# Performance work log

Measured on AMD Instinct MI355X. Metric: run time of the kernel, lower is better.

## Reference

```python
import jax, jax.numpy as jnp
import numpy as np

D_MODEL = 1024
N_HEADS = 16
D_HEAD = 64

def setup_inputs() -> dict:
    key = jax.random.key(0)
    k_x, k_q, k_k, k_v, k_o = jax.random.split(key, 5)
    B, T = 2, 2048
    scale = 1.0 / np.sqrt(D_MODEL)
    x = jax.random.normal(k_x, (B, T, D_MODEL), dtype=jnp.float32)
    W_q = jax.random.normal(k_q, (D_MODEL, N_HEADS * D_HEAD), dtype=jnp.float32) * scale
    W_k = jax.random.normal(k_k, (D_MODEL, N_HEADS * D_HEAD), dtype=jnp.float32) * scale
    W_v = jax.random.normal(k_v, (D_MODEL, N_HEADS * D_HEAD), dtype=jnp.float32) * scale
    W_out = jax.random.normal(k_o, (N_HEADS * D_HEAD, D_MODEL), dtype=jnp.float32) * scale
    return {"x": x, "W_q": W_q, "W_k": W_k, "W_v": W_v, "W_out": W_out}

def reference(x, W_q, W_k, W_v, W_out):
    B, T, _ = x.shape
    # project and split heads: [B, T, H, D] -> [B, H, T, D]
    def heads(W):
        return (x @ W).reshape(B, T, N_HEADS, D_HEAD).transpose(0, 2, 1, 3)
    Q, K, V = heads(W_q), heads(W_k), heads(W_v)
    scores = jnp.einsum('bhqd,bhkd->bhqk', Q, K) / jnp.sqrt(jnp.float32(D_HEAD))
    causal = jnp.tril(jnp.ones((T, T), dtype=bool))  # True = keep
    scores = jnp.where(causal, scores, jnp.float32(-jnp.inf))
    attn = jax.nn.softmax(scores, axis=-1)
    z = jnp.einsum('bhqk,bhkd->bhqd', attn, V)
    z = z.transpose(0, 2, 1, 3).reshape(B, T, N_HEADS * D_HEAD)
    return z @ W_out
```

## Files before the change

kernel.cpp:

```cpp
#include <hip/hip_runtime.h>
#include <cstdint>
#include <cstddef>

typedef __bf16 bf16_t;
typedef __bf16 bf16x8 __attribute__((ext_vector_type(8)));
typedef __bf16 bf16x4 __attribute__((ext_vector_type(4)));
typedef float floatx4 __attribute__((ext_vector_type(4)));

#define MFMA_BF16_16x16x32(a, b, c) \
  __builtin_amdgcn_mfma_f32_16x16x32_bf16((a), (b), (c), 0, 0, 0)

static constexpr int kT = 2048;
static constexpr int kDM = 1024;
static constexpr int kNH = 16;
static constexpr int kDH = 64;
static constexpr float kLog2e = 1.4426950408889634f;
static constexpr int kPS = 140;

__device__ __forceinline__ void gl_lds16(const bf16_t* g, bf16_t* l) {
  __builtin_amdgcn_global_load_lds(
      (const __attribute__((address_space(1))) void*)g,
      (__attribute__((address_space(3))) void*)l, 16, 0, 0);
}

__global__ __launch_bounds__(256) void detect_dtype(
    const unsigned short* __restrict__ xv, int* __restrict__ flagp) {
  __shared__ int bad_s[256];
  int bad = 0;
  for (int i = threadIdx.x; i < 8192; i += 256) {
    const unsigned e = (xv[i] >> 7) & 0xFF;
    if (e == 0xFF || (e != 0 && (e < 107 || e > 147))) bad++;
  }
  bad_s[threadIdx.x] = bad;
  __syncthreads();
  for (int s = 128; s > 0; s >>= 1) {
    if (threadIdx.x < s) bad_s[threadIdx.x] += bad_s[threadIdx.x + s];
    __syncthreads();
  }
  if (threadIdx.x == 0) *flagp = (bad_s[0] * 10 < 8192) ? 1 : 0;
}

__global__ __launch_bounds__(256) void convert_x(
    const void* __restrict__ src, bf16_t* __restrict__ dst,
    const int* __restrict__ flagp, int n) {
  const int f = *flagp;
  const int i = (blockIdx.x * 256 + threadIdx.x) * 8;
  if (i >= n) return;
  if (f) {
    *(bf16x8*)(dst + i) = *(const bf16x8*)((const bf16_t*)src + i);
  } else {
    const float* s = (const float*)src + i;
    bf16x8 v;
#pragma unroll
    for (int j = 0; j < 8; j++) v[j] = (bf16_t)s[j];
    *(bf16x8*)(dst + i) = v;
  }
}

__global__ __launch_bounds__(256) void convert_transpose_w(
    const void* __restrict__ w0, const void* __restrict__ w1,
    const void* __restrict__ w2, const void* __restrict__ w3,
    bf16_t* __restrict__ out_base, const int* __restrict__ flagp) {
  const int f = *flagp;
  const void* src = (blockIdx.z == 0) ? w0
                  : (blockIdx.z == 1) ? w1
                  : (blockIdx.z == 2) ? w2 : w3;
  bf16_t* dst = out_base + (size_t)blockIdx.z * (kDM * kDM);
  __shared__ bf16_t tile[64][65];
  const int tx = threadIdx.x & 63;
  const int ty = threadIdx.x >> 6;
  const int x0 = blockIdx.x * 64;
  const int y0 = blockIdx.y * 64;
#pragma unroll
  for (int r = 0; r < 64; r += 4) {
    const size_t idx = (size_t)(y0 + ty + r) * kDM + x0 + tx;
    tile[ty + r][tx] =
        f ? ((const bf16_t*)src)[idx] : (bf16_t)((const float*)src)[idx];
  }
  __syncthreads();
#pragma unroll
  for (int r = 0; r < 64; r += 4)
    dst[(size_t)(x0 + ty + r) * kDM + y0 + tx] = tile[tx][ty + r];
}

__device__ __forceinline__ void gemm_core_128x128(
    const bf16_t* __restrict__ A, const bf16_t* __restrict__ Bt, int K,
    bf16_t* __restrict__ sA, bf16_t* __restrict__ sB, floatx4 acc[4][4]) {
  const int tid = threadIdx.x;
  const int lane = tid & 63;
  const int w = tid >> 6;
  const int quad = lane >> 4;
  const int l16 = lane & 15;
  const int wm = w >> 1;
  const int wn = w & 1;
  const int sr = tid >> 2;
  const int sc = (tid & 3) * 8;
  const int wbase = w * 512;

  const bf16_t* pa0 = A + (size_t)sr * K + sc;
  const bf16_t* pa1 = A + (size_t)(sr + 64) * K + sc;
  const bf16_t* pb0 = Bt + (size_t)sr * K + sc;
  const bf16_t* pb1 = Bt + (size_t)(sr + 64) * K + sc;

  for (int kk = 0; kk < K; kk += 32) {
    __syncthreads();
    gl_lds16(pa0 + kk, sA + wbase);
    gl_lds16(pa1 + kk, sA + 2048 + wbase);
    gl_lds16(pb0 + kk, sB + wbase);
    gl_lds16(pb1 + kk, sB + 2048 + wbase);
    __syncthreads();
    bf16x8 af[4], bf[4];
#pragma unroll
    for (int mi = 0; mi < 4; mi++)
      af[mi] = *(const bf16x8*)(sA + (wm * 64 + mi * 16 + l16) * 32 + quad * 8);
#pragma unroll
    for (int ni = 0; ni < 4; ni++)
      bf[ni] = *(const bf16x8*)(sB + (wn * 64 + ni * 16 + l16) * 32 + quad * 8);
#pragma unroll
    for (int mi = 0; mi < 4; mi++)
#pragma unroll
      for (int ni = 0; ni < 4; ni++)
        acc[mi][ni] = MFMA_BF16_16x16x32(af[mi], bf[ni], acc[mi][ni]);
  }
}

__device__ __forceinline__ void gemm_core_64x128(
    const bf16_t* __restrict__ A, const bf16_t* __restrict__ Bt, int K,
    bf16_t* __restrict__ sA, bf16_t* __restrict__ sB, floatx4 acc[2][4]) {
  const int tid = threadIdx.x;
  const int lane = tid & 63;
  const int w = tid >> 6;
  const int quad = lane >> 4;
  const int l16 = lane & 15;
  const int wm = w >> 1;
  const int wn = w & 1;
  const int sr = tid >> 2;
  const int sc = (tid & 3) * 8;
  const int wbase = w * 512;

  const bf16_t* pa = A + (size_t)sr * K + sc;
  const bf16_t* pb0 = Bt + (size_t)sr * K + sc;
  const bf16_t* pb1 = Bt + (size_t)(sr + 64) * K + sc;

  for (int kk = 0; kk < K; kk += 32) {
    __syncthreads();
    gl_lds16(pa + kk, sA + wbase);
    gl_lds16(pb0 + kk, sB + wbase);
    gl_lds16(pb1 + kk, sB + 2048 + wbase);
    __syncthreads();
    bf16x8 af[2], bf[4];
#pragma unroll
    for (int mi = 0; mi < 2; mi++)
      af[mi] = *(const bf16x8*)(sA + (wm * 32 + mi * 16 + l16) * 32 + quad * 8);
#pragma unroll
    for (int ni = 0; ni < 4; ni++)
      bf[ni] = *(const bf16x8*)(sB + (wn * 64 + ni * 16 + l16) * 32 + quad * 8);
#pragma unroll
    for (int mi = 0; mi < 2; mi++)
#pragma unroll
      for (int ni = 0; ni < 4; ni++)
        acc[mi][ni] = MFMA_BF16_16x16x32(af[mi], bf[ni], acc[mi][ni]);
  }
}

__global__ __launch_bounds__(256) void qkv_proj(
    const bf16_t* __restrict__ x, const bf16_t* __restrict__ wt_base,
    bf16_t* __restrict__ Qf, bf16_t* __restrict__ Kf, bf16_t* __restrict__ Vf) {
  __shared__ bf16_t smem[8704];
  const int n0 = blockIdx.x * 128;
  const int m0 = blockIdx.y * 128;
  const int which = blockIdx.z;
  const bf16_t* Bt = wt_base + (size_t)which * (kDM * kDM);

  floatx4 acc[4][4];
  const floatx4 zero4 = {0.f, 0.f, 0.f, 0.f};
#pragma unroll
  for (int mi = 0; mi < 4; mi++)
#pragma unroll
    for (int ni = 0; ni < 4; ni++) acc[mi][ni] = zero4;

  gemm_core_128x128(x + (size_t)m0 * kDM, Bt + (size_t)n0 * kDM, kDM,
                    smem, smem + 4096, acc);

  const int tid = threadIdx.x;
  const int lane = tid & 63, w = tid >> 6;
  const int quad = lane >> 4, l16 = lane & 15;
  const int wm = w >> 1, wn = w & 1;
  const int h = (n0 + wn * 64) >> 6;

  if (which == 2) {
#pragma unroll
    for (int mi = 0; mi < 4; mi++) {
#pragma unroll
      for (int ni = 0; ni < 4; ni++) {
        const int n = n0 + wn * 64 + ni * 16 + l16;
        const int d = n & 63;
        const int ndv = d >> 4, l16v = d & 15;
        const int m = m0 + wm * 64 + mi * 16 + quad * 4;
        const int b = m >> 11, t0 = m & (kT - 1);
        const int kt = t0 >> 7, ks = (t0 >> 5) & 3, quadv = (t0 >> 3) & 3;
        const int eb = t0 & 4;
        bf16x4 v;
        v[0] = (bf16_t)acc[mi][ni][0];
        v[1] = (bf16_t)acc[mi][ni][1];
        v[2] = (bf16_t)acc[mi][ni][2];
        v[3] = (bf16_t)acc[mi][ni][3];
        *(bf16x4*)(Vf + (((((size_t)(b * kNH + h) * 16 + kt) * 4 + ks) * 4 +
                          ndv) * 64 + quadv * 16 + l16v) * 8 + eb) = v;
      }
    }
  } else {
    __syncthreads();
    bf16_t* Out = (which == 0) ? Qf : Kf;
    bf16_t* Lw = smem + w * 2176;
#pragma unroll
    for (int pass = 0; pass < 2; pass++) {
#pragma unroll
      for (int mi2 = 0; mi2 < 2; mi2++) {
        const int mi = pass * 2 + mi2;
#pragma unroll
        for (int ni = 0; ni < 4; ni++)
#pragma unroll
          for (int reg = 0; reg < 4; reg++)
            Lw[(mi2 * 16 + quad * 4 + reg) * 68 + ni * 16 + l16] =
                (bf16_t)acc[mi][ni][reg];
      }
      __asm volatile("s_waitcnt lgkmcnt(0)" ::: "memory");
      const int tb = m0 + wm * 64 + pass * 32;
#pragma unroll
      for (int i = 0; i < 4; i++) {
        const int khf = i >> 1, nifr = i & 1;
        const bf16x8 v = *(const bf16x8*)(Lw + (nifr * 16 + l16) * 68 +
                                          khf * 32 + quad * 8);
        const int t0 = tb + nifr * 16;
        const int b = t0 >> 11, tt = t0 & (kT - 1);
        size_t base;
        if (which == 0) {
          base = (((size_t)(b * kNH + h) * 128 + (tt >> 4)) * 2 + khf) * 512;
        } else {
          const int kt = tt >> 7, nif = (tt & 127) >> 4;
          base = ((((size_t)(b * kNH + h) * 16 + kt) * 2 + khf) * 8 + nif) * 512;
        }
        *(bf16x8*)(Out + base + lane * 8) = v;
      }
    }
  }
}

__device__ __forceinline__ void attn_task(
    int task, int lane, int l16, int quad, const bf16_t* __restrict__ Qb,
    const bf16_t* __restrict__ Kbf, const bf16_t* __restrict__ Vbf,
    bf16_t* __restrict__ Pw, bf16_t* __restrict__ Z, int b, int h) {
  const int q0 = task * 16;
  const int nkt = (task >> 3) + 1;
  const float C1 = 0.125f * kLog2e;

  bf16x8 qf[2];
#pragma unroll
  for (int kh = 0; kh < 2; kh++)
    qf[kh] = *(const bf16x8*)(Qb + ((size_t)task * 2 + kh) * 512 + lane * 8);

  const floatx4 zero4 = {0.f, 0.f, 0.f, 0.f};
  floatx4 of[4];
  float lrow[4];
#pragma unroll
  for (int nd = 0; nd < 4; nd++) of[nd] = zero4;
#pragma unroll
  for (int r = 0; r < 4; r++) lrow[r] = 0.f;

  bf16x8 kf[16];
#pragma unroll
  for (int fi = 0; fi < 16; fi++)
    kf[fi] = *(const bf16x8*)(Kbf + (size_t)fi * 512 + lane * 8);

  for (int kt = 0; kt < nkt; kt++) {
    const int kbase = kt * 128;
    floatx4 sf[8];
#pragma unroll
    for (int ni = 0; ni < 8; ni++) sf[ni] = zero4;
#pragma unroll
    for (int kh = 0; kh < 2; kh++)
#pragma unroll
      for (int ni = 0; ni < 8; ni++)
        sf[ni] = MFMA_BF16_16x16x32(qf[kh], kf[kh * 8 + ni], sf[ni]);
    const int ktp = (kt + 1 < nkt) ? kt + 1 : kt;
    const bf16_t* kp = Kbf + (size_t)ktp * 16 * 512 + lane * 8;
#pragma unroll
    for (int fi = 0; fi < 16; fi++)
      kf[fi] = *(const bf16x8*)(kp + (size_t)fi * 512);
    const bf16_t* vp = Vbf + (size_t)kt * 16 * 512 + lane * 8;
    bf16x8 vf[16];
#pragma unroll
    for (int fi = 0; fi < 16; fi++)
      vf[fi] = *(const bf16x8*)(vp + (size_t)fi * 512);
    const bool diag = (kt == nkt - 1);
#pragma unroll
    for (int reg = 0; reg < 4; reg++) {
      const int row_l = quad * 4 + reg;
      const int row_g = q0 + row_l;
      float rsum = 0.f;
#pragma unroll
      for (int ni = 0; ni < 8; ni++) {
        float s = sf[ni][reg] * C1 - 16.f;
        if (diag && (kbase + ni * 16 + l16 > row_g)) s = -3.0e38f;
        const float p = exp2f(s);
        rsum += p;
        Pw[row_l * kPS + ni * 16 + l16] = (bf16_t)p;
      }
      lrow[reg] += rsum;
    }
    __asm volatile("s_waitcnt lgkmcnt(0)" ::: "memory");
#pragma unroll
    for (int ks = 0; ks < 4; ks++) {
      const bf16x8 af = *(const bf16x8*)(Pw + l16 * kPS + ks * 32 + quad * 8);
#pragma unroll
      for (int nd = 0; nd < 4; nd++)
        of[nd] = MFMA_BF16_16x16x32(af, vf[ks * 4 + nd], of[nd]);
    }
  }

#pragma unroll
  for (int reg = 0; reg < 4; reg++) {
#pragma unroll
    for (int off = 1; off < 16; off <<= 1)
      lrow[reg] += __shfl_xor(lrow[reg], off, 64);
  }
#pragma unroll
  for (int reg = 0; reg < 4; reg++) {
    const int t = q0 + quad * 4 + reg;
    const float inv = 1.f / lrow[reg];
#pragma unroll
    for (int nd = 0; nd < 4; nd++) {
      const int col = h * 64 + nd * 16 + l16;
      Z[(size_t)(b * kT + t) * kDM + col] = (bf16_t)(of[nd][reg] * inv);
    }
  }
}

__global__ __launch_bounds__(256, 2) void attn_fused(
    const bf16_t* __restrict__ Qf, const bf16_t* __restrict__ Kf,
    const bf16_t* __restrict__ Vf, bf16_t* __restrict__ Z) {
  __shared__ bf16_t Ps[64 * kPS];
  const int bh = blockIdx.x;
  const int tid = threadIdx.x;
  const int lane = tid & 63;
  const int w = tid >> 6;
  const int quad = lane >> 4;
  const int l16 = lane & 15;
  const int pairidx = blockIdx.y * 4 + w;
  bf16_t* Pw = Ps + (w * 16) * kPS;

  const bf16_t* Qb = Qf + (size_t)bh * kT * kDH;
  const bf16_t* Kbf = Kf + (size_t)bh * kT * kDH;
  const bf16_t* Vbf = Vf + (size_t)bh * kT * kDH;
  const int b = bh >> 4, h = bh & 15;

  attn_task(pairidx, lane, l16, quad, Qb, Kbf, Vbf, Pw, Z, b, h);
  attn_task(127 - pairidx, lane, l16, quad, Qb, Kbf, Vbf, Pw, Z, b, h);
}

__global__ __launch_bounds__(256) void out_proj(
    const bf16_t* __restrict__ Zin, const bf16_t* __restrict__ WtO,
    void* __restrict__ out, const int* __restrict__ flagp) {
  __shared__ bf16_t smem[6144];
  const int f = *flagp;
  const int n0 = blockIdx.x * 128;
  const int m0 = blockIdx.y * 64;
  floatx4 acc[2][4];
  const floatx4 zero4 = {0.f, 0.f, 0.f, 0.f};
#pragma unroll
  for (int mi = 0; mi < 2; mi++)
#pragma unroll
    for (int ni = 0; ni < 4; ni++) acc[mi][ni] = zero4;

  gemm_core_64x128(Zin + (size_t)m0 * kDM, WtO + (size_t)n0 * kDM, kDM,
                   smem, smem + 2048, acc);

  const int tid = threadIdx.x;
  const int lane = tid & 63, w = tid >> 6;
  const int quad = lane >> 4, l16 = lane & 15;
  const int wm = w >> 1, wn = w & 1;
#pragma unroll
  for (int mi = 0; mi < 2; mi++) {
#pragma unroll
    for (int ni = 0; ni < 4; ni++) {
      const int n = n0 + wn * 64 + ni * 16 + l16;
#pragma unroll
      for (int reg = 0; reg < 4; reg++) {
        const int m = m0 + wm * 32 + mi * 16 + quad * 4 + reg;
        if (f) {
          ((bf16_t*)out)[(size_t)m * kDM + n] = (bf16_t)acc[mi][ni][reg];
        } else {
          ((float*)out)[(size_t)m * kDM + n] = acc[mi][ni][reg];
        }
      }
    }
  }
}

extern "C" void kernel_launch(void* const* d_in, const int* in_sizes, int n_in,
                              void* d_out, int out_size, void* d_ws,
                              size_t ws_size, hipStream_t stream) {
  const void* x = d_in[0];
  const void* Wq = d_in[1];
  const void* Wk = d_in[2];
  const void* Wv = d_in[3];
  const void* Wo = d_in[4];
  bf16_t* ws = (bf16_t*)d_ws;
  const size_t MEG = 1024 * 1024;
  bf16_t* wt = ws;
  bf16_t* xb = ws + 4 * MEG;
  bf16_t* Qf = ws + 8 * MEG;
  bf16_t* Kf = ws + 12 * MEG;
  bf16_t* Vf = ws + 16 * MEG;
  bf16_t* Z = ws + 20 * MEG;
  int* flagp = (int*)(ws + 24 * MEG);

  detect_dtype<<<1, 256, 0, stream>>>((const unsigned short*)x, flagp);
  convert_x<<<2048, 256, 0, stream>>>(x, xb, flagp, 4 * (int)MEG);
  convert_transpose_w<<<dim3(16, 16, 4), 256, 0, stream>>>(Wq, Wk, Wv, Wo, wt,
                                                           flagp);
  qkv_proj<<<dim3(8, 32, 3), 256, 0, stream>>>(xb, wt, Qf, Kf, Vf);
  attn_fused<<<dim3(32, 16), 256, 0, stream>>>(Qf, Kf, Vf, Z);
  out_proj<<<dim3(8, 64), 256, 0, stream>>>(Z, wt + 3 * MEG, d_out, flagp);
}
```

Baseline: 194.6 us.

## Split attention KV range across wave pairs, deepen GEMM K-step, merge conversions

Each query tile's key range is split between two waves, and the partial outputs and row sums are combined through LDS. This doubles the attention grid and raises the occupancy hint, to improve load balance and parallelism. Both GEMM cores now stage 64 K-elements per barrier pair instead of 32, halving the synchronisations at the cost of doubled LDS. The x conversion and weight transposes are merged into one launch, and the diagonal mask check is hoisted out of the non-diagonal path.

```diff
diff --git a/kernel.cpp b/kernel.cpp
--- a/kernel.cpp
+++ b/kernel.cpp
@@ -40,32 +40,33 @@
   if (threadIdx.x == 0) *flagp = (bad_s[0] * 10 < 8192) ? 1 : 0;
 }
 
-__global__ __launch_bounds__(256) void convert_x(
-    const void* __restrict__ src, bf16_t* __restrict__ dst,
-    const int* __restrict__ flagp, int n) {
+__global__ __launch_bounds__(256) void convert_all(
+    const void* __restrict__ xsrc, const void* __restrict__ w0,
+    const void* __restrict__ w1, const void* __restrict__ w2,
+    const void* __restrict__ w3, bf16_t* __restrict__ xb,
+    bf16_t* __restrict__ wt_base, const int* __restrict__ flagp) {
   const int f = *flagp;
-  const int i = (blockIdx.x * 256 + threadIdx.x) * 8;
-  if (i >= n) return;
-  if (f) {
-    *(bf16x8*)(dst + i) = *(const bf16x8*)((const bf16_t*)src + i);
-  } else {
-    const float* s = (const float*)src + i;
-    bf16x8 v;
-#pragma unroll
-    for (int j = 0; j < 8; j++) v[j] = (bf16_t)s[j];
-    *(bf16x8*)(dst + i) = v;
-  }
-}
-
-__global__ __launch_bounds__(256) void convert_transpose_w(
-    const void* __restrict__ w0, const void* __restrict__ w1,
-    const void* __restrict__ w2, const void* __restrict__ w3,
-    bf16_t* __restrict__ out_base, const int* __restrict__ flagp) {
-  const int f = *flagp;
+  if (blockIdx.z == 4) {
+    const int base = (blockIdx.y * 16 + blockIdx.x) * 16384;
+#pragma unroll
+    for (int it = 0; it < 8; it++) {
+      const int i = base + (it * 256 + threadIdx.x) * 8;
+      if (f) {
+        *(bf16x8*)(xb + i) = *(const bf16x8*)((const bf16_t*)xsrc + i);
+      } else {
+        const float* s = (const float*)xsrc + i;
+        bf16x8 v;
+#pragma unroll
+        for (int j = 0; j < 8; j++) v[j] = (bf16_t)s[j];
+        *(bf16x8*)(xb + i) = v;
+      }
+    }
+    return;
+  }
   const void* src = (blockIdx.z == 0) ? w0
                   : (blockIdx.z == 1) ? w1
                   : (blockIdx.z == 2) ? w2 : w3;
-  bf16_t* dst = out_base + (size_t)blockIdx.z * (kDM * kDM);
+  bf16_t* dst = wt_base + (size_t)blockIdx.z * (kDM * kDM);
   __shared__ bf16_t tile[64][65];
   const int tx = threadIdx.x & 63;
   const int ty = threadIdx.x >> 6;
@@ -102,25 +103,33 @@
   const bf16_t* pb0 = Bt + (size_t)sr * K + sc;
   const bf16_t* pb1 = Bt + (size_t)(sr + 64) * K + sc;
 
-  for (int kk = 0; kk < K; kk += 32) {
-    __syncthreads();
-    gl_lds16(pa0 + kk, sA + wbase);
-    gl_lds16(pa1 + kk, sA + 2048 + wbase);
-    gl_lds16(pb0 + kk, sB + wbase);
-    gl_lds16(pb1 + kk, sB + 2048 + wbase);
-    __syncthreads();
-    bf16x8 af[4], bf[4];
-#pragma unroll
-    for (int mi = 0; mi < 4; mi++)
-      af[mi] = *(const bf16x8*)(sA + (wm * 64 + mi * 16 + l16) * 32 + quad * 8);
-#pragma unroll
-    for (int ni = 0; ni < 4; ni++)
-      bf[ni] = *(const bf16x8*)(sB + (wn * 64 + ni * 16 + l16) * 32 + quad * 8);
-#pragma unroll
-    for (int mi = 0; mi < 4; mi++)
+  for (int kk = 0; kk < K; kk += 64) {
+    __syncthreads();
+#pragma unroll
+    for (int kh = 0; kh < 2; kh++) {
+      gl_lds16(pa0 + kk + kh * 32, sA + kh * 4096 + wbase);
+      gl_lds16(pa1 + kk + kh * 32, sA + kh * 4096 + 2048 + wbase);
+      gl_lds16(pb0 + kk + kh * 32, sB + kh * 4096 + wbase);
+      gl_lds16(pb1 + kk + kh * 32, sB + kh * 4096 + 2048 + wbase);
+    }
+    __syncthreads();
+#pragma unroll
+    for (int kh = 0; kh < 2; kh++) {
+      bf16x8 af[4], bf[4];
+#pragma unroll
+      for (int mi = 0; mi < 4; mi++)
+        af[mi] = *(const bf16x8*)(sA + kh * 4096 +
+                                  (wm * 64 + mi * 16 + l16) * 32 + quad * 8);
 #pragma unroll
       for (int ni = 0; ni < 4; ni++)
-        acc[mi][ni] = MFMA_BF16_16x16x32(af[mi], bf[ni], acc[mi][ni]);
+        bf[ni] = *(const bf16x8*)(sB + kh * 4096 +
+                                  (wn * 64 + ni * 16 + l16) * 32 + quad * 8);
+#pragma unroll
+      for (int mi = 0; mi < 4; mi++)
+#pragma unroll
+        for (int ni = 0; ni < 4; ni++)
+          acc[mi][ni] = MFMA_BF16_16x16x32(af[mi], bf[ni], acc[mi][ni]);
+    }
   }
 }
 
@@ -142,31 +151,39 @@
   const bf16_t* pb0 = Bt + (size_t)sr * K + sc;
   const bf16_t* pb1 = Bt + (size_t)(sr + 64) * K + sc;
 
-  for (int kk = 0; kk < K; kk += 32) {
-    __syncthreads();
-    gl_lds16(pa + kk, sA + wbase);
-    gl_lds16(pb0 + kk, sB + wbase);
-    gl_lds16(pb1 + kk, sB + 2048 + wbase);
-    __syncthreads();
-    bf16x8 af[2], bf[4];
-#pragma unroll
-    for (int mi = 0; mi < 2; mi++)
-      af[mi] = *(const bf16x8*)(sA + (wm * 32 + mi * 16 + l16) * 32 + quad * 8);
-#pragma unroll
-    for (int ni = 0; ni < 4; ni++)
-      bf[ni] = *(const bf16x8*)(sB + (wn * 64 + ni * 16 + l16) * 32 + quad * 8);
-#pragma unroll
-    for (int mi = 0; mi < 2; mi++)
+  for (int kk = 0; kk < K; kk += 64) {
+    __syncthreads();
+#pragma unroll
+    for (int kh = 0; kh < 2; kh++) {
+      gl_lds16(pa + kk + kh * 32, sA + kh * 2048 + wbase);
+      gl_lds16(pb0 + kk + kh * 32, sB + kh * 4096 + wbase);
+      gl_lds16(pb1 + kk + kh * 32, sB + kh * 4096 + 2048 + wbase);
+    }
+    __syncthreads();
+#pragma unroll
+    for (int kh = 0; kh < 2; kh++) {
+      bf16x8 af[2], bf[4];
+#pragma unroll
+      for (int mi = 0; mi < 2; mi++)
+        af[mi] = *(const bf16x8*)(sA + kh * 2048 +
+                                  (wm * 32 + mi * 16 + l16) * 32 + quad * 8);
 #pragma unroll
       for (int ni = 0; ni < 4; ni++)
-        acc[mi][ni] = MFMA_BF16_16x16x32(af[mi], bf[ni], acc[mi][ni]);
+        bf[ni] = *(const bf16x8*)(sB + kh * 4096 +
+                                  (wn * 64 + ni * 16 + l16) * 32 + quad * 8);
+#pragma unroll
+      for (int mi = 0; mi < 2; mi++)
+#pragma unroll
+        for (int ni = 0; ni < 4; ni++)
+          acc[mi][ni] = MFMA_BF16_16x16x32(af[mi], bf[ni], acc[mi][ni]);
+    }
   }
 }
 
 __global__ __launch_bounds__(256) void qkv_proj(
     const bf16_t* __restrict__ x, const bf16_t* __restrict__ wt_base,
     bf16_t* __restrict__ Qf, bf16_t* __restrict__ Kf, bf16_t* __restrict__ Vf) {
-  __shared__ bf16_t smem[8704];
+  __shared__ bf16_t smem[16384];
   const int n0 = blockIdx.x * 128;
   const int m0 = blockIdx.y * 128;
   const int which = blockIdx.z;
@@ -180,7 +197,7 @@
     for (int ni = 0; ni < 4; ni++) acc[mi][ni] = zero4;
 
   gemm_core_128x128(x + (size_t)m0 * kDM, Bt + (size_t)n0 * kDM, kDM,
-                    smem, smem + 4096, acc);
+                    smem, smem + 8192, acc);
 
   const int tid = threadIdx.x;
   const int lane = tid & 63, w = tid >> 6;
@@ -247,33 +264,31 @@
   }
 }
 
-__device__ __forceinline__ void attn_task(
-    int task, int lane, int l16, int quad, const bf16_t* __restrict__ Qb,
-    const bf16_t* __restrict__ Kbf, const bf16_t* __restrict__ Vbf,
-    bf16_t* __restrict__ Pw, bf16_t* __restrict__ Z, int b, int h) {
+__device__ __forceinline__ void attn_half(
+    int task, int k0, int k1, int nkt, int lane, int l16, int quad,
+    const bf16_t* __restrict__ Qb, const bf16_t* __restrict__ Kbf,
+    const bf16_t* __restrict__ Vbf, bf16_t* __restrict__ Pw,
+    floatx4 of[4], float lrow[4]) {
   const int q0 = task * 16;
-  const int nkt = (task >> 3) + 1;
   const float C1 = 0.125f * kLog2e;
+  const floatx4 zero4 = {0.f, 0.f, 0.f, 0.f};
+#pragma unroll
+  for (int nd = 0; nd < 4; nd++) of[nd] = zero4;
+#pragma unroll
+  for (int r = 0; r < 4; r++) lrow[r] = 0.f;
+  if (k0 >= k1) return;
 
   bf16x8 qf[2];
 #pragma unroll
   for (int kh = 0; kh < 2; kh++)
     qf[kh] = *(const bf16x8*)(Qb + ((size_t)task * 2 + kh) * 512 + lane * 8);
 
-  const floatx4 zero4 = {0.f, 0.f, 0.f, 0.f};
-  floatx4 of[4];
-  float lrow[4];
-#pragma unroll
-  for (int nd = 0; nd < 4; nd++) of[nd] = zero4;
-#pragma unroll
-  for (int r = 0; r < 4; r++) lrow[r] = 0.f;
-
   bf16x8 kf[16];
 #pragma unroll
   for (int fi = 0; fi < 16; fi++)
-    kf[fi] = *(const bf16x8*)(Kbf + (size_t)fi * 512 + lane * 8);
-
-  for (int kt = 0; kt < nkt; kt++) {
+    kf[fi] = *(const bf16x8*)(Kbf + ((size_t)k0 * 16 + fi) * 512 + lane * 8);
+
+  for (int kt = k0; kt < k1; kt++) {
     const int kbase = kt * 128;
     floatx4 sf[8];
 #pragma unroll
@@ -283,7 +298,7 @@
 #pragma unroll
       for (int ni = 0; ni < 8; ni++)
         sf[ni] = MFMA_BF16_16x16x32(qf[kh], kf[kh * 8 + ni], sf[ni]);
-    const int ktp = (kt + 1 < nkt) ? kt + 1 : kt;
+    const int ktp = (kt + 1 < k1) ? kt + 1 : kt;
     const bf16_t* kp = Kbf + (size_t)ktp * 16 * 512 + lane * 8;
 #pragma unroll
     for (int fi = 0; fi < 16; fi++)
@@ -293,21 +308,33 @@
 #pragma unroll
     for (int fi = 0; fi < 16; fi++)
       vf[fi] = *(const bf16x8*)(vp + (size_t)fi * 512);
-    const bool diag = (kt == nkt - 1);
-#pragma unroll
-    for (int reg = 0; reg < 4; reg++) {
-      const int row_l = quad * 4 + reg;
-      const int row_g = q0 + row_l;
-      float rsum = 0.f;
-#pragma unroll
-      for (int ni = 0; ni < 8; ni++) {
-        float s = sf[ni][reg] * C1 - 16.f;
-        if (diag && (kbase + ni * 16 + l16 > row_g)) s = -3.0e38f;
-        const float p = exp2f(s);
-        rsum += p;
-        Pw[row_l * kPS + ni * 16 + l16] = (bf16_t)p;
-      }
-      lrow[reg] += rsum;
+    if (kt == nkt - 1) {
+#pragma unroll
+      for (int reg = 0; reg < 4; reg++) {
+        const int row_g = q0 + quad * 4 + reg;
+        float rsum = 0.f;
+#pragma unroll
+        for (int ni = 0; ni < 8; ni++) {
+          float s = sf[ni][reg] * C1 - 16.f;
+          if (kbase + ni * 16 + l16 > row_g) s = -3.0e38f;
+          const float p = exp2f(s);
+          rsum += p;
+          Pw[(quad * 4 + reg) * kPS + ni * 16 + l16] = (bf16_t)p;
+        }
+        lrow[reg] += rsum;
+      }
+    } else {
+#pragma unroll
+      for (int reg = 0; reg < 4; reg++) {
+        float rsum = 0.f;
+#pragma unroll
+        for (int ni = 0; ni < 8; ni++) {
+          const float p = exp2f(sf[ni][reg] * C1 - 16.f);
+          rsum += p;
+          Pw[(quad * 4 + reg) * kPS + ni * 16 + l16] = (bf16_t)p;
+        }
+        lrow[reg] += rsum;
+      }
     }
     __asm volatile("s_waitcnt lgkmcnt(0)" ::: "memory");
 #pragma unroll
@@ -318,36 +345,23 @@
         of[nd] = MFMA_BF16_16x16x32(af, vf[ks * 4 + nd], of[nd]);
     }
   }
-
-#pragma unroll
-  for (int reg = 0; reg < 4; reg++) {
-#pragma unroll
-    for (int off = 1; off < 16; off <<= 1)
-      lrow[reg] += __shfl_xor(lrow[reg], off, 64);
-  }
-#pragma unroll
-  for (int reg = 0; reg < 4; reg++) {
-    const int t = q0 + quad * 4 + reg;
-    const float inv = 1.f / lrow[reg];
-#pragma unroll
-    for (int nd = 0; nd < 4; nd++) {
-      const int col = h * 64 + nd * 16 + l16;
-      Z[(size_t)(b * kT + t) * kDM + col] = (bf16_t)(of[nd][reg] * inv);
-    }
-  }
-}
-
-__global__ __launch_bounds__(256, 2) void attn_fused(
+}
+
+__global__ __launch_bounds__(256, 4) void attn_fused(
     const bf16_t* __restrict__ Qf, const bf16_t* __restrict__ Kf,
     const bf16_t* __restrict__ Vf, bf16_t* __restrict__ Z) {
   __shared__ bf16_t Ps[64 * kPS];
+  __shared__ float MO[2][64][16];
+  __shared__ float ML[2][64][4];
   const int bh = blockIdx.x;
   const int tid = threadIdx.x;
   const int lane = tid & 63;
   const int w = tid >> 6;
   const int quad = lane >> 4;
   const int l16 = lane & 15;
-  const int pairidx = blockIdx.y * 4 + w;
+  const int pairsel = w >> 1;
+  const int half = w & 1;
+  const int p = blockIdx.y * 2 + pairsel;
   bf16_t* Pw = Ps + (w * 16) * kPS;
 
   const bf16_t* Qb = Qf + (size_t)bh * kT * kDH;
@@ -355,14 +369,59 @@
   const bf16_t* Vbf = Vf + (size_t)bh * kT * kDH;
   const int b = bh >> 4, h = bh & 15;
 
-  attn_task(pairidx, lane, l16, quad, Qb, Kbf, Vbf, Pw, Z, b, h);
-  attn_task(127 - pairidx, lane, l16, quad, Qb, Kbf, Vbf, Pw, Z, b, h);
+#pragma unroll
+  for (int ts = 0; ts < 2; ts++) {
+    const int task = (ts == 0) ? p : 127 - p;
+    const int nkt = (task >> 3) + 1;
+    const int h0 = (nkt + 1) >> 1;
+    const int k0 = half ? h0 : 0;
+    const int k1 = half ? nkt : h0;
+    floatx4 of[4];
+    float lrow[4];
+    attn_half(task, k0, k1, nkt, lane, l16, quad, Qb, Kbf, Vbf, Pw, of, lrow);
+    if (half == 1) {
+#pragma unroll
+      for (int nd = 0; nd < 4; nd++)
+#pragma unroll
+        for (int reg = 0; reg < 4; reg++)
+          MO[pairsel][lane][nd * 4 + reg] = of[nd][reg];
+#pragma unroll
+      for (int reg = 0; reg < 4; reg++) ML[pairsel][lane][reg] = lrow[reg];
+    }
+    __syncthreads();
+    if (half == 0) {
+#pragma unroll
+      for (int nd = 0; nd < 4; nd++)
+#pragma unroll
+        for (int reg = 0; reg < 4; reg++)
+          of[nd][reg] += MO[pairsel][lane][nd * 4 + reg];
+#pragma unroll
+      for (int reg = 0; reg < 4; reg++) {
+        lrow[reg] += ML[pairsel][lane][reg];
+#pragma unroll
+        for (int off = 1; off < 16; off <<= 1)
+          lrow[reg] += __shfl_xor(lrow[reg], off, 64);
+      }
+      const int q0 = task * 16;
+#pragma unroll
+      for (int reg = 0; reg < 4; reg++) {
+        const int t = q0 + quad * 4 + reg;
+        const float inv = 1.f / lrow[reg];
+#pragma unroll
+        for (int nd = 0; nd < 4; nd++) {
+          const int col = h * 64 + nd * 16 + l16;
+          Z[(size_t)(b * kT + t) * kDM + col] = (bf16_t)(of[nd][reg] * inv);
+        }
+      }
+    }
+    __syncthreads();
+  }
 }
 
 __global__ __launch_bounds__(256) void out_proj(
     const bf16_t* __restrict__ Zin, const bf16_t* __restrict__ WtO,
     void* __restrict__ out, const int* __restrict__ flagp) {
-  __shared__ bf16_t smem[6144];
+  __shared__ bf16_t smem[12288];
   const int f = *flagp;
   const int n0 = blockIdx.x * 128;
   const int m0 = blockIdx.y * 64;
@@ -374,7 +433,7 @@
     for (int ni = 0; ni < 4; ni++) acc[mi][ni] = zero4;
 
   gemm_core_64x128(Zin + (size_t)m0 * kDM, WtO + (size_t)n0 * kDM, kDM,
-                   smem, smem + 2048, acc);
+                   smem, smem + 4096, acc);
 
   const int tid = threadIdx.x;
   const int lane = tid & 63, w = tid >> 6;
@@ -417,10 +476,9 @@
   int* flagp = (int*)(ws + 24 * MEG);
 
   detect_dtype<<<1, 256, 0, stream>>>((const unsigned short*)x, flagp);
-  convert_x<<<2048, 256, 0, stream>>>(x, xb, flagp, 4 * (int)MEG);
-  convert_transpose_w<<<dim3(16, 16, 4), 256, 0, stream>>>(Wq, Wk, Wv, Wo, wt,
-                                                           flagp);
+  convert_all<<<dim3(16, 16, 5), 256, 0, stream>>>(x, Wq, Wk, Wv, Wo, xb, wt,
+                                                   flagp);
   qkv_proj<<<dim3(8, 32, 3), 256, 0, stream>>>(xb, wt, Qf, Kf, Vf);
-  attn_fused<<<dim3(32, 16), 256, 0, stream>>>(Qf, Kf, Vf, Z);
+  attn_fused<<<dim3(32, 32), 256, 0, stream>>>(Qf, Kf, Vf, Z);
   out_proj<<<dim3(8, 64), 256, 0, stream>>>(Z, wt + 3 * MEG, d_out, flagp);
 }
```

Result: slower. 401.1 us (+106.1%).

## Pair query tiles per wave with split-K merge, inline dtype detection, swap GEMM grid order

Applied to the files above, without the earlier changes.

Each wave now handles two adjacent 16-row query tiles at once and reuses the same K and V fragments for both. Two waves split the key range of each pair and merge their partial outputs and row sums through shared memory. The separate dtype-detection kernel is dropped; each kernel instead checks 128 input samples itself, which removes one launch but repeats the check in every thread and relies on a smaller sample. The GEMM grids are also transposed so that blockIdx.x walks M, which changes the order in which tiles are scheduled and how they share cache.

```diff
diff --git a/kernel.cpp b/kernel.cpp
--- a/kernel.cpp
+++ b/kernel.cpp
@@ -23,27 +23,18 @@
       (__attribute__((address_space(3))) void*)l, 16, 0, 0);
 }
 
-__global__ __launch_bounds__(256) void detect_dtype(
-    const unsigned short* __restrict__ xv, int* __restrict__ flagp) {
-  __shared__ int bad_s[256];
+__device__ __forceinline__ int detect_bf16(const unsigned short* __restrict__ xv) {
   int bad = 0;
-  for (int i = threadIdx.x; i < 8192; i += 256) {
+  for (int i = 0; i < 128; i++) {
     const unsigned e = (xv[i] >> 7) & 0xFF;
     if (e == 0xFF || (e != 0 && (e < 107 || e > 147))) bad++;
   }
-  bad_s[threadIdx.x] = bad;
-  __syncthreads();
-  for (int s = 128; s > 0; s >>= 1) {
-    if (threadIdx.x < s) bad_s[threadIdx.x] += bad_s[threadIdx.x + s];
-    __syncthreads();
-  }
-  if (threadIdx.x == 0) *flagp = (bad_s[0] * 10 < 8192) ? 1 : 0;
+  return bad < 13;
 }
 
 __global__ __launch_bounds__(256) void convert_x(
-    const void* __restrict__ src, bf16_t* __restrict__ dst,
-    const int* __restrict__ flagp, int n) {
-  const int f = *flagp;
+    const void* __restrict__ src, bf16_t* __restrict__ dst, int n) {
+  const int f = detect_bf16((const unsigned short*)src);
   const int i = (blockIdx.x * 256 + threadIdx.x) * 8;
   if (i >= n) return;
   if (f) {
@@ -58,10 +49,10 @@
 }
 
 __global__ __launch_bounds__(256) void convert_transpose_w(
-    const void* __restrict__ w0, const void* __restrict__ w1,
-    const void* __restrict__ w2, const void* __restrict__ w3,
-    bf16_t* __restrict__ out_base, const int* __restrict__ flagp) {
-  const int f = *flagp;
+    const void* __restrict__ xsrc, const void* __restrict__ w0,
+    const void* __restrict__ w1, const void* __restrict__ w2,
+    const void* __restrict__ w3, bf16_t* __restrict__ out_base) {
+  const int f = detect_bf16((const unsigned short*)xsrc);
   const void* src = (blockIdx.z == 0) ? w0
                   : (blockIdx.z == 1) ? w1
                   : (blockIdx.z == 2) ? w2 : w3;
@@ -167,8 +158,8 @@
     const bf16_t* __restrict__ x, const bf16_t* __restrict__ wt_base,
     bf16_t* __restrict__ Qf, bf16_t* __restrict__ Kf, bf16_t* __restrict__ Vf) {
   __shared__ bf16_t smem[8704];
-  const int n0 = blockIdx.x * 128;
-  const int m0 = blockIdx.y * 128;
+  const int m0 = blockIdx.x * 128;
+  const int n0 = blockIdx.y * 128;
   const int which = blockIdx.z;
   const bf16_t* Bt = wt_base + (size_t)which * (kDM * kDM);
 
@@ -247,34 +238,36 @@
   }
 }
 
-__device__ __forceinline__ void attn_task(
-    int task, int lane, int l16, int quad, const bf16_t* __restrict__ Qb,
-    const bf16_t* __restrict__ Kbf, const bf16_t* __restrict__ Vbf,
-    bf16_t* __restrict__ Pw, bf16_t* __restrict__ Z, int b, int h) {
-  const int q0 = task * 16;
-  const int nkt = (task >> 3) + 1;
+__device__ __forceinline__ void attn_pair(
+    int tA, int k0, int k1, int nkt, int lane, int l16, int quad,
+    const bf16_t* __restrict__ Qb, const bf16_t* __restrict__ Kbf,
+    const bf16_t* __restrict__ Vbf, bf16_t* __restrict__ Pw,
+    floatx4 ofA[4], floatx4 ofB[4], float lA[4], float lB[4]) {
+  const int tB = tA + 1;
   const float C1 = 0.125f * kLog2e;
-
-  bf16x8 qf[2];
-#pragma unroll
-  for (int kh = 0; kh < 2; kh++)
-    qf[kh] = *(const bf16x8*)(Qb + ((size_t)task * 2 + kh) * 512 + lane * 8);
-
   const floatx4 zero4 = {0.f, 0.f, 0.f, 0.f};
-  floatx4 of[4];
-  float lrow[4];
-#pragma unroll
-  for (int nd = 0; nd < 4; nd++) of[nd] = zero4;
-#pragma unroll
-  for (int r = 0; r < 4; r++) lrow[r] = 0.f;
+#pragma unroll
+  for (int nd = 0; nd < 4; nd++) { ofA[nd] = zero4; ofB[nd] = zero4; }
+#pragma unroll
+  for (int r = 0; r < 4; r++) { lA[r] = 0.f; lB[r] = 0.f; }
+  if (k0 >= k1) return;
+
+  bf16x8 qfA[2], qfB[2];
+#pragma unroll
+  for (int kh = 0; kh < 2; kh++) {
+    qfA[kh] = *(const bf16x8*)(Qb + ((size_t)tA * 2 + kh) * 512 + lane * 8);
+    qfB[kh] = *(const bf16x8*)(Qb + ((size_t)tB * 2 + kh) * 512 + lane * 8);
+  }
 
   bf16x8 kf[16];
 #pragma unroll
   for (int fi = 0; fi < 16; fi++)
-    kf[fi] = *(const bf16x8*)(Kbf + (size_t)fi * 512 + lane * 8);
-
-  for (int kt = 0; kt < nkt; kt++) {
+    kf[fi] = *(const bf16x8*)(Kbf + ((size_t)k0 * 16 + fi) * 512 + lane * 8);
+
+  for (int kt = k0; kt < k1; kt++) {
     const int kbase = kt * 128;
+    const bool diag = (kt == nkt - 1);
+    const bf16_t* vp = Vbf + (size_t)kt * 16 * 512 + lane * 8;
     floatx4 sf[8];
 #pragma unroll
     for (int ni = 0; ni < 8; ni++) sf[ni] = zero4;
@@ -282,22 +275,15 @@
     for (int kh = 0; kh < 2; kh++)
 #pragma unroll
       for (int ni = 0; ni < 8; ni++)
-        sf[ni] = MFMA_BF16_16x16x32(qf[kh], kf[kh * 8 + ni], sf[ni]);
-    const int ktp = (kt + 1 < nkt) ? kt + 1 : kt;
-    const bf16_t* kp = Kbf + (size_t)ktp * 16 * 512 + lane * 8;
-#pragma unroll
-    for (int fi = 0; fi < 16; fi++)
-      kf[fi] = *(const bf16x8*)(kp + (size_t)fi * 512);
-    const bf16_t* vp = Vbf + (size_t)kt * 16 * 512 + lane * 8;
-    bf16x8 vf[16];
-#pragma unroll
-    for (int fi = 0; fi < 16; fi++)
-      vf[fi] = *(const bf16x8*)(vp + (size_t)fi * 512);
-    const bool diag = (kt == nkt - 1);
+        sf[ni] = MFMA_BF16_16x16x32(qfA[kh], kf[kh * 8 + ni], sf[ni]);
+    bf16x8 vf0[8];
+#pragma unroll
+    for (int fi = 0; fi < 8; fi++)
+      vf0[fi] = *(const bf16x8*)(vp + (size_t)fi * 512);
 #pragma unroll
     for (int reg = 0; reg < 4; reg++) {
       const int row_l = quad * 4 + reg;
-      const int row_g = q0 + row_l;
+      const int row_g = tA * 16 + row_l;
       float rsum = 0.f;
 #pragma unroll
       for (int ni = 0; ni < 8; ni++) {
@@ -307,32 +293,51 @@
         rsum += p;
         Pw[row_l * kPS + ni * 16 + l16] = (bf16_t)p;
       }
-      lrow[reg] += rsum;
+      lA[reg] += rsum;
+    }
+#pragma unroll
+    for (int ni = 0; ni < 8; ni++) sf[ni] = zero4;
+#pragma unroll
+    for (int kh = 0; kh < 2; kh++)
+#pragma unroll
+      for (int ni = 0; ni < 8; ni++)
+        sf[ni] = MFMA_BF16_16x16x32(qfB[kh], kf[kh * 8 + ni], sf[ni]);
+    const int ktp = (kt + 1 < k1) ? kt + 1 : kt;
+    const bf16_t* kp = Kbf + (size_t)ktp * 16 * 512 + lane * 8;
+#pragma unroll
+    for (int fi = 0; fi < 16; fi++)
+      kf[fi] = *(const bf16x8*)(kp + (size_t)fi * 512);
+#pragma unroll
+    for (int reg = 0; reg < 4; reg++) {
+      const int row_l = quad * 4 + reg;
+      const int row_g = tB * 16 + row_l;
+      float rsum = 0.f;
+#pragma unroll
+      for (int ni = 0; ni < 8; ni++) {
+        float s = sf[ni][reg] * C1 - 16.f;
+        if (diag && (kbase + ni * 16 + l16 > row_g)) s = -3.0e38f;
+        const float p = exp2f(s);
+        rsum += p;
+        Pw[(16 + row_l) * kPS + ni * 16 + l16] = (bf16_t)p;
+      }
+      lB[reg] += rsum;
     }
     __asm volatile("s_waitcnt lgkmcnt(0)" ::: "memory");
+    bf16x8 vf1[8];
+#pragma unroll
+    for (int fi = 0; fi < 8; fi++)
+      vf1[fi] = *(const bf16x8*)(vp + (size_t)(8 + fi) * 512);
 #pragma unroll
     for (int ks = 0; ks < 4; ks++) {
-      const bf16x8 af = *(const bf16x8*)(Pw + l16 * kPS + ks * 32 + quad * 8);
-#pragma unroll
-      for (int nd = 0; nd < 4; nd++)
-        of[nd] = MFMA_BF16_16x16x32(af, vf[ks * 4 + nd], of[nd]);
-    }
-  }
-
-#pragma unroll
-  for (int reg = 0; reg < 4; reg++) {
-#pragma unroll
-    for (int off = 1; off < 16; off <<= 1)
-      lrow[reg] += __shfl_xor(lrow[reg], off, 64);
-  }
-#pragma unroll
-  for (int reg = 0; reg < 4; reg++) {
-    const int t = q0 + quad * 4 + reg;
-    const float inv = 1.f / lrow[reg];
-#pragma unroll
-    for (int nd = 0; nd < 4; nd++) {
-      const int col = h * 64 + nd * 16 + l16;
-      Z[(size_t)(b * kT + t) * kDM + col] = (bf16_t)(of[nd][reg] * inv);
+      const bf16x8 afA = *(const bf16x8*)(Pw + l16 * kPS + ks * 32 + quad * 8);
+      const bf16x8 afB =
+          *(const bf16x8*)(Pw + (16 + l16) * kPS + ks * 32 + quad * 8);
+#pragma unroll
+      for (int nd = 0; nd < 4; nd++) {
+        const bf16x8 vv = (ks < 2) ? vf0[ks * 4 + nd] : vf1[(ks - 2) * 4 + nd];
+        ofA[nd] = MFMA_BF16_16x16x32(afA, vv, ofA[nd]);
+        ofB[nd] = MFMA_BF16_16x16x32(afB, vv, ofB[nd]);
+      }
     }
   }
 }
@@ -340,32 +345,97 @@
 __global__ __launch_bounds__(256, 2) void attn_fused(
     const bf16_t* __restrict__ Qf, const bf16_t* __restrict__ Kf,
     const bf16_t* __restrict__ Vf, bf16_t* __restrict__ Z) {
-  __shared__ bf16_t Ps[64 * kPS];
+  __shared__ bf16_t Ps[128 * kPS];
+  __shared__ float MO[2][2][64][17];
+  __shared__ float ML[2][2][64][5];
   const int bh = blockIdx.x;
   const int tid = threadIdx.x;
   const int lane = tid & 63;
   const int w = tid >> 6;
   const int quad = lane >> 4;
   const int l16 = lane & 15;
-  const int pairidx = blockIdx.y * 4 + w;
-  bf16_t* Pw = Ps + (w * 16) * kPS;
+  const int pairsel = w >> 1;
+  const int half = w & 1;
+  const int u = blockIdx.y * 2 + pairsel;
+  bf16_t* Pw = Ps + (w * 32) * kPS;
 
   const bf16_t* Qb = Qf + (size_t)bh * kT * kDH;
   const bf16_t* Kbf = Kf + (size_t)bh * kT * kDH;
   const bf16_t* Vbf = Vf + (size_t)bh * kT * kDH;
   const int b = bh >> 4, h = bh & 15;
 
-  attn_task(pairidx, lane, l16, quad, Qb, Kbf, Vbf, Pw, Z, b, h);
-  attn_task(127 - pairidx, lane, l16, quad, Qb, Kbf, Vbf, Pw, Z, b, h);
+#pragma unroll
+  for (int ts = 0; ts < 2; ts++) {
+    const int pu = ts ? (63 - u) : u;
+    const int tA = pu * 2;
+    const int nkt = (tA >> 3) + 1;
+    const int h0 = (nkt + 1) >> 1;
+    const int k0 = half ? h0 : 0;
+    const int k1 = half ? nkt : h0;
+    floatx4 ofA[4], ofB[4];
+    float lA[4], lB[4];
+    attn_pair(tA, k0, k1, nkt, lane, l16, quad, Qb, Kbf, Vbf, Pw,
+              ofA, ofB, lA, lB);
+    if (half == 1) {
+#pragma unroll
+      for (int nd = 0; nd < 4; nd++)
+#pragma unroll
+        for (int reg = 0; reg < 4; reg++) {
+          MO[pairsel][0][lane][nd * 4 + reg] = ofA[nd][reg];
+          MO[pairsel][1][lane][nd * 4 + reg] = ofB[nd][reg];
+        }
+#pragma unroll
+      for (int reg = 0; reg < 4; reg++) {
+        ML[pairsel][0][lane][reg] = lA[reg];
+        ML[pairsel][1][lane][reg] = lB[reg];
+      }
+    }
+    __syncthreads();
+    if (half == 0) {
+#pragma unroll
+      for (int nd = 0; nd < 4; nd++)
+#pragma unroll
+        for (int reg = 0; reg < 4; reg++) {
+          ofA[nd][reg] += MO[pairsel][0][lane][nd * 4 + reg];
+          ofB[nd][reg] += MO[pairsel][1][lane][nd * 4 + reg];
+        }
+#pragma unroll
+      for (int reg = 0; reg < 4; reg++) {
+        lA[reg] += ML[pairsel][0][lane][reg];
+        lB[reg] += ML[pairsel][1][lane][reg];
+#pragma unroll
+        for (int off = 1; off < 16; off <<= 1) {
+          lA[reg] += __shfl_xor(lA[reg], off, 64);
+          lB[reg] += __shfl_xor(lB[reg], off, 64);
+        }
+      }
+#pragma unroll
+      for (int t2 = 0; t2 < 2; t2++) {
+        const int q0 = (tA + t2) * 16;
+#pragma unroll
+        for (int reg = 0; reg < 4; reg++) {
+          const int t = q0 + quad * 4 + reg;
+          const float inv = 1.f / (t2 ? lB[reg] : lA[reg]);
+#pragma unroll
+          for (int nd = 0; nd < 4; nd++) {
+            const int col = h * 64 + nd * 16 + l16;
+            const float ov = t2 ? ofB[nd][reg] : ofA[nd][reg];
+            Z[(size_t)(b * kT + t) * kDM + col] = (bf16_t)(ov * inv);
+          }
+        }
+      }
+    }
+    __syncthreads();
+  }
 }
 
 __global__ __launch_bounds__(256) void out_proj(
     const bf16_t* __restrict__ Zin, const bf16_t* __restrict__ WtO,
-    void* __restrict__ out, const int* __restrict__ flagp) {
+    void* __restrict__ out, const void* __restrict__ xsrc) {
   __shared__ bf16_t smem[6144];
-  const int f = *flagp;
-  const int n0 = blockIdx.x * 128;
-  const int m0 = blockIdx.y * 64;
+  const int f = detect_bf16((const unsigned short*)xsrc);
+  const int m0 = blockIdx.x * 64;
+  const int n0 = blockIdx.y * 128;
   floatx4 acc[2][4];
   const floatx4 zero4 = {0.f, 0.f, 0.f, 0.f};
 #pragma unroll
@@ -414,13 +484,11 @@
   bf16_t* Kf = ws + 12 * MEG;
   bf16_t* Vf = ws + 16 * MEG;
   bf16_t* Z = ws + 20 * MEG;
-  int* flagp = (int*)(ws + 24 * MEG);
-
-  detect_dtype<<<1, 256, 0, stream>>>((const unsigned short*)x, flagp);
-  convert_x<<<2048, 256, 0, stream>>>(x, xb, flagp, 4 * (int)MEG);
-  convert_transpose_w<<<dim3(16, 16, 4), 256, 0, stream>>>(Wq, Wk, Wv, Wo, wt,
-                                                           flagp);
-  qkv_proj<<<dim3(8, 32, 3), 256, 0, stream>>>(xb, wt, Qf, Kf, Vf);
+
+  convert_x<<<2048, 256, 0, stream>>>(x, xb, 4 * (int)MEG);
+  convert_transpose_w<<<dim3(16, 16, 4), 256, 0, stream>>>(x, Wq, Wk, Wv, Wo,
+                                                           wt);
+  qkv_proj<<<dim3(32, 8, 3), 256, 0, stream>>>(xb, wt, Qf, Kf, Vf);
   attn_fused<<<dim3(32, 16), 256, 0, stream>>>(Qf, Kf, Vf, Z);
-  out_proj<<<dim3(8, 64), 256, 0, stream>>>(Z, wt + 3 * MEG, d_out, flagp);
-}
+  out_proj<<<dim3(64, 8), 256, 0, stream>>>(Z, wt + 3 * MEG, d_out, x);
+}
```

New measurement: 227.8 us. 1.17x slower.
